# Kernel tuning notes

Measured on AMD Instinct MI355X. Metric: run time of the kernel, lower is better.

## Reference

```python
import jax, jax.numpy as jnp
import numpy as np

DIM = 192
HEADS = 8
EPS = 1e-12

def conv2d(x, w, groups=1, padding='SAME'):
    return jax.lax.conv_general_dilated(
        x, w, window_strides=(1, 1), padding=padding,
        dimension_numbers=('NCHW', 'OIHW', 'NCHW'),
        feature_group_count=groups)

def setup_inputs() -> dict:
    key = jax.random.key(0)
    ks = jax.random.split(key, 6)
    b, c, h, w = 8, DIM, 128, 128
    x = jax.random.normal(ks[0], (b, c, h, w), dtype=jnp.float32)
    # depthwise 3x3 conv on x (groups=dim): OIHW with I=1
    w_dw = jax.random.normal(ks[1], (DIM, 1, 3, 3), dtype=jnp.float32) * 0.1
    # 1x1 qkv projection
    w_qkv = jax.random.normal(ks[2], (DIM * 3, DIM, 1, 1), dtype=jnp.float32) * (1.0 / np.sqrt(DIM))
    # depthwise 3x3 on qkv (groups=3*dim)
    w_qkvdw = jax.random.normal(ks[3], (DIM * 3, 1, 3, 3), dtype=jnp.float32) * 0.1
    # 1x1 output projection
    w_proj = jax.random.normal(ks[4], (DIM, DIM, 1, 1), dtype=jnp.float32) * (1.0 / np.sqrt(DIM))
    temperature = jnp.ones((HEADS, 1, 1), dtype=jnp.float32)
    rescale = jnp.ones((HEADS, 1), dtype=jnp.float32)
    return {"x": x, "w_dw": w_dw, "w_qkv": w_qkv, "w_qkvdw": w_qkvdw,
            "w_proj": w_proj, "temperature": temperature, "rescale": rescale}

def l2norm_lastdim(t):
    # matches F.normalize(t, dim=-1, eps=1e-12)
    n = jnp.sqrt(jnp.sum(t * t, axis=-1, keepdims=True))
    return t / jnp.maximum(n, EPS)

def reference(x, w_dw, w_qkv, w_qkvdw, w_proj, temperature, rescale):
    b, c, h, w = x.shape
    heads = HEADS
    c_head = c // heads
    # variance (unbiased, like torch.var default) of depthwise-conv features over H,W
    xd = conv2d(x, w_dw, groups=c)                      # [b,c,h,w]
    var = jnp.var(xd, axis=(-2, -1), ddof=1)            # [b,c]
    var = var.reshape(b, heads, c_head)                 # [b,head,c_head]
    # qkv: 1x1 conv then depthwise 3x3
    qkv = conv2d(conv2d(x, w_qkv), w_qkvdw, groups=3 * c)  # [b,3c,h,w]
    q, k, v = jnp.split(qkv, 3, axis=1)
    def to_heads(t):
        return t.reshape(b, heads, c_head, h * w)       # b head c (h w)
    q, k, v = to_heads(q), to_heads(k), to_heads(v)
    q = l2norm_lastdim(q)
    k = l2norm_lastdim(k)
    # channel attention: [b,head,c_head,c_head]
    attn = jnp.einsum('bhcn,bhdn->bhcd', q, k) * temperature
    # diagonal bias from variance, scaled per-head
    diag = rescale * var                                # [b,head,c_head]
    attn = attn + jnp.einsum('bhc,cd->bhcd', diag, jnp.eye(c_head, dtype=attn.dtype))
    attn = jax.nn.softmax(attn, axis=-1)
    out = jnp.einsum('bhcd,bhdn->bhcn', attn, v)        # [b,head,c_head,hw]
    out = out.reshape(b, c, h, w)
    return conv2d(out, w_proj)
```

## Files before the change

### kernel.cpp

```cpp
#include <hip/hip_runtime.h>
#include <hip/hip_bf16.h>

typedef unsigned short ushort_t;
typedef __bf16 bf16x8 __attribute__((ext_vector_type(8)));
typedef float f32x4 __attribute__((ext_vector_type(4)));
typedef unsigned short us8 __attribute__((ext_vector_type(8)));
typedef unsigned short us4 __attribute__((ext_vector_type(4)));

#define HW 16384
#define CDIM 192
#define QKVC 576

static __device__ __forceinline__ float b2f(unsigned short u) {
    union { unsigned int i; float f; } cv; cv.i = ((unsigned int)u) << 16; return cv.f;
}
static __device__ __forceinline__ unsigned short f2b(float f) {
    union { __bf16 h; unsigned short u; } cv; cv.h = (__bf16)f; return cv.u;
}

__global__ __launch_bounds__(256) void k_cvt(const float* __restrict__ src,
                                             ushort_t* __restrict__ dst, int n8) {
    int i = blockIdx.x * 256 + threadIdx.x;
    if (i >= n8) return;
    f32x4 a = *(const f32x4*)&src[i * 8];
    f32x4 b = *(const f32x4*)&src[i * 8 + 4];
    us8 o;
#pragma unroll
    for (int e = 0; e < 4; ++e) { o[e] = f2b(a[e]); o[4 + e] = f2b(b[e]); }
    *(us8*)&dst[i * 8] = o;
}

__global__ __launch_bounds__(256) void k_dwvar(const float* __restrict__ x,
                                               const float* __restrict__ wdw,
                                               float* __restrict__ vs1,
                                               float* __restrict__ vs2,
                                               ushort_t* __restrict__ xb) {
    __shared__ __align__(16) float pl[66 * 132];
    __shared__ float red[8];
    int blk = blockIdx.x;
    int bc = blk >> 1, half = blk & 1, rb = half * 64;
    int c = bc % CDIM;
    const float* xp = x + (size_t)bc * HW;
    ushort_t* xbp = xb + (size_t)bc * HW;
    int t = threadIdx.x;
#pragma unroll
    for (int i = 0; i < 8; ++i) {
        int gi = t + i * 256;
        int row = gi >> 5, q4 = (gi & 31) * 4;
        f32x4 v4 = *(const f32x4*)&xp[(size_t)(rb + row) * 128 + q4];
        *(f32x4*)&pl[(row + 1) * 132 + q4] = v4;
        us4 b4;
#pragma unroll
        for (int j = 0; j < 4; ++j) b4[j] = f2b(v4[j]);
        *(us4*)&xbp[(size_t)(rb + row) * 128 + q4] = b4;
    }
    if (t < 32) {
        f32x4 v = {0.f, 0.f, 0.f, 0.f};
        if (rb > 0) v = *(const f32x4*)&xp[(size_t)(rb - 1) * 128 + t * 4];
        *(f32x4*)&pl[t * 4] = v;
    } else if (t < 64) {
        int g = t - 32;
        f32x4 v = {0.f, 0.f, 0.f, 0.f};
        if (rb + 64 < 128) v = *(const f32x4*)&xp[(size_t)(rb + 64) * 128 + g * 4];
        *(f32x4*)&pl[65 * 132 + g * 4] = v;
    }
    float w[9];
#pragma unroll
    for (int j = 0; j < 9; ++j) w[j] = wdw[c * 9 + j];
    __syncthreads();

    int lane = t & 63, wv = t >> 6;
    int y = lane, xs = wv * 32;
    int yb0 = y * 132, yb1 = yb0 + 132, yb2 = yb1 + 132;
    float l0 = 0.f, l1 = 0.f, l2 = 0.f;
    if (xs != 0) { l0 = pl[yb0 + xs - 1]; l1 = pl[yb1 + xs - 1]; l2 = pl[yb2 + xs - 1]; }
    float s1 = 0.f, s2 = 0.f;
#pragma unroll
    for (int g = 0; g < 4; ++g) {
        int x0 = xs + g * 8;
        float e0[10], e1[10], e2[10];
        e0[0] = l0; e1[0] = l1; e2[0] = l2;
        f32x4 a0 = *(const f32x4*)&pl[yb0 + x0], b0 = *(const f32x4*)&pl[yb0 + x0 + 4];
        f32x4 a1 = *(const f32x4*)&pl[yb1 + x0], b1 = *(const f32x4*)&pl[yb1 + x0 + 4];
        f32x4 a2 = *(const f32x4*)&pl[yb2 + x0], b2 = *(const f32x4*)&pl[yb2 + x0 + 4];
#pragma unroll
        for (int j = 0; j < 4; ++j) {
            e0[1 + j] = a0[j]; e0[5 + j] = b0[j];
            e1[1 + j] = a1[j]; e1[5 + j] = b1[j];
            e2[1 + j] = a2[j]; e2[5 + j] = b2[j];
        }
        float r0v = 0.f, r1v = 0.f, r2v = 0.f;
        if (x0 + 8 < 128) { r0v = pl[yb0 + x0 + 8]; r1v = pl[yb1 + x0 + 8]; r2v = pl[yb2 + x0 + 8]; }
        e0[9] = r0v; e1[9] = r1v; e2[9] = r2v;
#pragma unroll
        for (int j = 0; j < 8; ++j) {
            float o = e0[j] * w[0] + e0[j + 1] * w[1] + e0[j + 2] * w[2]
                    + e1[j] * w[3] + e1[j + 1] * w[4] + e1[j + 2] * w[5]
                    + e2[j] * w[6] + e2[j + 1] * w[7] + e2[j + 2] * w[8];
            s1 += o; s2 += o * o;
        }
        l0 = e0[8]; l1 = e1[8]; l2 = e2[8];
    }
#pragma unroll
    for (int off = 32; off; off >>= 1) { s1 += __shfl_xor(s1, off); s2 += __shfl_xor(s2, off); }
    if (lane == 0) { red[wv * 2] = s1; red[wv * 2 + 1] = s2; }
    __syncthreads();
    if (t == 0) {
        atomicAdd(&vs1[bc], red[0] + red[2] + red[4] + red[6]);
        atomicAdd(&vs2[bc], red[1] + red[3] + red[5] + red[7]);
    }
}

__global__ __launch_bounds__(256) void k_dwqkv(const ushort_t* __restrict__ qkvraw,
                                               const float* __restrict__ wqd,
                                               ushort_t* __restrict__ qkvd,
                                               float* __restrict__ ssq) {
    __shared__ __align__(16) ushort_t pl[66 * 136];
    __shared__ float red[4];
    int blk = blockIdx.x;
    int bo = blk >> 1, half = blk & 1, rb = half * 64;
    int o = bo % QKVC, b = bo / QKVC;
    const ushort_t* xp = qkvraw + (size_t)bo * HW;
    ushort_t* op = qkvd + (size_t)bo * HW;
    int t = threadIdx.x;
#pragma unroll
    for (int i = 0; i < 4; ++i) {
        int gi = t + i * 256;
        int row = gi >> 4, gr = (gi & 15) * 8;
        *(us8*)&pl[(row + 1) * 136 + gr] = *(const us8*)&xp[(size_t)(rb + row) * 128 + gr];
    }
    if (t < 16) {
        us8 v = {};
        if (rb > 0) v = *(const us8*)&xp[(size_t)(rb - 1) * 128 + t * 8];
        *(us8*)&pl[t * 8] = v;
    } else if (t < 32) {
        int g = t - 16;
        us8 v = {};
        if (rb + 64 < 128) v = *(const us8*)&xp[(size_t)(rb + 64) * 128 + g * 8];
        *(us8*)&pl[65 * 136 + g * 8] = v;
    }
    float w[9];
#pragma unroll
    for (int j = 0; j < 9; ++j) w[j] = wqd[o * 9 + j];
    __syncthreads();

    int lane = t & 63, wv = t >> 6;
    int y = lane, xs = wv * 32;
    int yb0 = y * 136, yb1 = yb0 + 136, yb2 = yb1 + 136;
    float l0 = 0.f, l1 = 0.f, l2 = 0.f;
    if (xs != 0) { l0 = b2f(pl[yb0 + xs - 1]); l1 = b2f(pl[yb1 + xs - 1]); l2 = b2f(pl[yb2 + xs - 1]); }
    float s2 = 0.f;
#pragma unroll
    for (int g = 0; g < 4; ++g) {
        int x0 = xs + g * 8;
        us8 v0 = *(const us8*)&pl[yb0 + x0];
        us8 v1 = *(const us8*)&pl[yb1 + x0];
        us8 v2 = *(const us8*)&pl[yb2 + x0];
        float r0v = 0.f, r1v = 0.f, r2v = 0.f;
        if (x0 + 8 < 128) { r0v = b2f(pl[yb0 + x0 + 8]); r1v = b2f(pl[yb1 + x0 + 8]); r2v = b2f(pl[yb2 + x0 + 8]); }
        float e0[10], e1[10], e2[10];
        e0[0] = l0; e1[0] = l1; e2[0] = l2;
#pragma unroll
        for (int j = 0; j < 8; ++j) { e0[j + 1] = b2f(v0[j]); e1[j + 1] = b2f(v1[j]); e2[j + 1] = b2f(v2[j]); }
        e0[9] = r0v; e1[9] = r1v; e2[9] = r2v;
        us8 ob;
#pragma unroll
        for (int j = 0; j < 8; ++j) {
            float ov = e0[j] * w[0] + e0[j + 1] * w[1] + e0[j + 2] * w[2]
                     + e1[j] * w[3] + e1[j + 1] * w[4] + e1[j + 2] * w[5]
                     + e2[j] * w[6] + e2[j + 1] * w[7] + e2[j + 2] * w[8];
            unsigned short bits = f2b(ov);
            ob[j] = bits;
            float rv = b2f(bits);
            s2 += rv * rv;
        }
        *(us8*)&op[(size_t)(rb + y) * 128 + x0] = ob;
        l0 = e0[8]; l1 = e1[8]; l2 = e2[8];
    }
#pragma unroll
    for (int off = 32; off; off >>= 1) s2 += __shfl_xor(s2, off);
    if (lane == 0) red[wv] = s2;
    __syncthreads();
    if (t == 0 && o < 2 * CDIM)
        atomicAdd(&ssq[b * 384 + o], red[0] + red[1] + red[2] + red[3]);
}

template<int CF>
__global__ __launch_bounds__(256) void k_gemm(const ushort_t* __restrict__ Av, long sAb,
                                              const ushort_t* __restrict__ Bv, long sBb,
                                              void* __restrict__ Cv, long sCb, int K) {
    __shared__ __align__(16) char smem[49152];
    ushort_t* As = (ushort_t*)smem;
    ushort_t* Bs = (ushort_t*)(smem + 24576);
    int t = threadIdx.x;
    int wv = t >> 6, lane = t & 63, quad = lane >> 4, l15 = lane & 15;
    size_t aoff = (size_t)blockIdx.z * sAb + (size_t)blockIdx.y * 192 * K;
    size_t boff = (size_t)blockIdx.z * sBb + (size_t)blockIdx.x * 128;
    size_t coff = (size_t)blockIdx.z * sCb + (size_t)blockIdx.y * 192 * HW + (size_t)blockIdx.x * 128;
    f32x4 acc[24] = {};
    int bkr = t >> 3, bn0 = (t & 7) * 16, tlow = t & 7;
    int gk0 = bkr >> 3, klo = bkr & 7;
    const ushort_t* Bp = Bv + boff;
    us8 pb0 = *(const us8*)&Bp[(size_t)bkr * HW + bn0];
    us8 pb1 = *(const us8*)&Bp[(size_t)bkr * HW + bn0 + 8];
    us8 pb2 = *(const us8*)&Bp[(size_t)(bkr + 32) * HW + bn0];
    us8 pb3 = *(const us8*)&Bp[(size_t)(bkr + 32) * HW + bn0 + 8];
    int nIter = K >> 6;
    for (int it = 0; it < nIter; ++it) {
        int kk = it << 6;
#pragma unroll
        for (int i = 0; i < 6; ++i) {
            int s = t + i * 256;
            int row = s >> 3, kc = (s & 7) * 8;
            int kcs = kc ^ ((row & 7) * 8);
            *(uint4*)&As[row * 64 + kcs] = *(const uint4*)&Av[aoff + (size_t)row * K + kk + kc];
        }
#pragma unroll
        for (int e = 0; e < 8; ++e) {
            int col0 = ((gk0 ^ tlow ^ e) << 3) + klo;
            Bs[(bn0 + e) * 64 + col0] = pb0[e];
            Bs[(bn0 + 8 + e) * 64 + col0] = pb1[e];
            int col1 = (((gk0 + 4) ^ tlow ^ e) << 3) + klo;
            Bs[(bn0 + e) * 64 + col1] = pb2[e];
            Bs[(bn0 + 8 + e) * 64 + col1] = pb3[e];
        }
        __syncthreads();
        if (it + 1 < nIter) {
            const ushort_t* Bn = &Bp[(size_t)(kk + 64) * HW];
            pb0 = *(const us8*)&Bn[(size_t)bkr * HW + bn0];
            pb1 = *(const us8*)&Bn[(size_t)bkr * HW + bn0 + 8];
            pb2 = *(const us8*)&Bn[(size_t)(bkr + 32) * HW + bn0];
            pb3 = *(const us8*)&Bn[(size_t)(bkr + 32) * HW + bn0 + 8];
        }
#pragma unroll
        for (int s = 0; s < 2; ++s) {
            int r0 = wv * 16 + l15, r1 = 64 + r0, r2 = 128 + r0;
            int ko = s * 32 + quad * 8;
            bf16x8 af0 = *(const bf16x8*)&As[r0 * 64 + (ko ^ ((r0 & 7) * 8))];
            bf16x8 af1 = *(const bf16x8*)&As[r1 * 64 + (ko ^ ((r1 & 7) * 8))];
            bf16x8 af2 = *(const bf16x8*)&As[r2 * 64 + (ko ^ ((r2 & 7) * 8))];
#pragma unroll
            for (int tc = 0; tc < 8; ++tc) {
                int n = tc * 16 + l15;
                int g = (s * 4 + quad) ^ ((tc ^ l15) & 7);
                bf16x8 bfr = *(const bf16x8*)&Bs[n * 64 + (g << 3)];
                acc[tc]      = __builtin_amdgcn_mfma_f32_16x16x32_bf16(af0, bfr, acc[tc],      0, 0, 0);
                acc[8 + tc]  = __builtin_amdgcn_mfma_f32_16x16x32_bf16(af1, bfr, acc[8 + tc],  0, 0, 0);
                acc[16 + tc] = __builtin_amdgcn_mfma_f32_16x16x32_bf16(af2, bfr, acc[16 + tc], 0, 0, 0);
            }
        }
        __syncthreads();
    }
    if (CF == 0) {
        ushort_t* Ct = (ushort_t*)smem;
#pragma unroll
        for (int rt = 0; rt < 3; ++rt)
#pragma unroll
            for (int tc = 0; tc < 8; ++tc)
#pragma unroll
                for (int r = 0; r < 4; ++r)
                    Ct[(rt * 64 + wv * 16 + quad * 4 + r) * 128 + tc * 16 + l15] = f2b(acc[rt * 8 + tc][r]);
        __syncthreads();
        ushort_t* Co = (ushort_t*)Cv;
#pragma unroll
        for (int i = 0; i < 12; ++i) {
            int s = t + i * 256;
            int row = s >> 4, c8 = (s & 15) * 8;
            *(us8*)&Co[coff + (size_t)row * HW + c8] = *(us8*)&Ct[row * 128 + c8];
        }
    } else {
        float* Cf = (float*)smem;
        float* Co = (float*)Cv;
#pragma unroll
        for (int rt = 0; rt < 3; ++rt) {
            if (rt) __syncthreads();
#pragma unroll
            for (int tc = 0; tc < 8; ++tc)
#pragma unroll
                for (int r = 0; r < 4; ++r)
                    Cf[(wv * 16 + quad * 4 + r) * 128 + tc * 16 + l15] = acc[rt * 8 + tc][r];
            __syncthreads();
#pragma unroll
            for (int i = 0; i < 8; ++i) {
                int s = t + i * 256;
                int row = s >> 5, c4 = (s & 31) * 4;
                *(f32x4*)&Co[coff + (size_t)(rt * 64 + row) * HW + c4] = *(f32x4*)&Cf[row * 128 + c4];
            }
        }
    }
}

__global__ __launch_bounds__(256) void k_gram(const ushort_t* __restrict__ qkvd,
                                              float* __restrict__ G) {
    __shared__ __align__(16) ushort_t qs[24 * 264];
    __shared__ __align__(16) ushort_t ks[24 * 264];
    int bh = blockIdx.y;
    int b = bh >> 3, h = bh & 7;
    int t = threadIdx.x, wv = t >> 6, lane = t & 63, quad = lane >> 4, l15 = lane & 15;
    const ushort_t* qb = qkvd + (size_t)b * 9437184 + (size_t)(h * 24) * HW;
    const ushort_t* kp = qb + (size_t)CDIM * HW;
    f32x4 a00 = {}, a01 = {}, a10 = {}, a11 = {};
    bf16x8 z = {};
    bool hi = (l15 < 8);
    int kbase0 = blockIdx.x * 2048;
    for (int sub = 0; sub < 8; ++sub) {
        int kbase = kbase0 + sub * 256;
#pragma unroll
        for (int j = 0; j < 3; ++j) {
            int gi = t + j * 256;
            int row = gi >> 5, c8 = (gi & 31) * 8;
            *(us8*)&qs[row * 264 + c8] = *(const us8*)&qb[(size_t)row * HW + kbase + c8];
            *(us8*)&ks[row * 264 + c8] = *(const us8*)&kp[(size_t)row * HW + kbase + c8];
        }
        __syncthreads();
#pragma unroll
        for (int s = 0; s < 2; ++s) {
            int ko = (wv * 2 + s) * 32 + quad * 8;
            bf16x8 qa0 = *(const bf16x8*)&qs[l15 * 264 + ko];
            bf16x8 qa1 = hi ? *(const bf16x8*)&qs[(16 + l15) * 264 + ko] : z;
            bf16x8 kb0 = *(const bf16x8*)&ks[l15 * 264 + ko];
            bf16x8 kb1 = hi ? *(const bf16x8*)&ks[(16 + l15) * 264 + ko] : z;
            a00 = __builtin_amdgcn_mfma_f32_16x16x32_bf16(qa0, kb0, a00, 0, 0, 0);
            a01 = __builtin_amdgcn_mfma_f32_16x16x32_bf16(qa0, kb1, a01, 0, 0, 0);
            a10 = __builtin_amdgcn_mfma_f32_16x16x32_bf16(qa1, kb0, a10, 0, 0, 0);
            a11 = __builtin_amdgcn_mfma_f32_16x16x32_bf16(qa1, kb1, a11, 0, 0, 0);
        }
        __syncthreads();
    }
    float* Gp = G + (size_t)bh * 576;
#pragma unroll
    for (int r = 0; r < 4; ++r) {
        int r0 = quad * 4 + r, r1 = 16 + quad * 4 + r;
        int c0 = l15, c1 = 16 + l15;
        atomicAdd(&Gp[r0 * 24 + c0], a00[r]);
        if (c1 < 24) atomicAdd(&Gp[r0 * 24 + c1], a01[r]);
        if (r1 < 24) atomicAdd(&Gp[r1 * 24 + c0], a10[r]);
        if (r1 < 24 && c1 < 24) atomicAdd(&Gp[r1 * 24 + c1], a11[r]);
    }
}

__global__ __launch_bounds__(256) void k_smweff(const float* __restrict__ G,
                                                const float* __restrict__ ssq,
                                                const float* __restrict__ vs1,
                                                const float* __restrict__ vs2,
                                                const float* __restrict__ wproj,
                                                const float* __restrict__ temp,
                                                const float* __restrict__ resc,
                                                ushort_t* __restrict__ Weff) {
    int b = blockIdx.x, t = threadIdx.x;
    __shared__ float P[8 * 24 * 24];
    __shared__ float snq[192], snk[192];
    if (t < 192) {
        snq[t] = fmaxf(sqrtf(ssq[b * 384 + t]), 1e-12f);
        snk[t] = fmaxf(sqrtf(ssq[b * 384 + 192 + t]), 1e-12f);
    }
    __syncthreads();
    if (t < 192) {
        int h = t / 24, c = t % 24;
        float tmpv = temp[h];
        float S1 = vs1[b * 192 + t], S2 = vs2[b * 192 + t];
        float varv = (S2 - S1 * S1 * (1.0f / 16384.f)) * (1.0f / 16383.f);
        float dvar = resc[h] * varv;
        const float* Gp = G + (size_t)(b * 8 + h) * 576 + c * 24;
        float inq = tmpv / snq[t];
        float lg[24]; float mx = -1e30f;
#pragma unroll
        for (int d = 0; d < 24; ++d) {
            float v = Gp[d] * inq / snk[h * 24 + d];
            if (d == c) v += dvar;
            lg[d] = v; mx = fmaxf(mx, v);
        }
        float sum = 0.f;
#pragma unroll
        for (int d = 0; d < 24; ++d) { float e = __expf(lg[d] - mx); lg[d] = e; sum += e; }
        float inv = 1.f / sum;
#pragma unroll
        for (int d = 0; d < 24; ++d) P[(h * 24 + c) * 24 + d] = lg[d] * inv;
    }
    __syncthreads();
#pragma unroll
    for (int i = 0; i < 6; ++i) {
        int idx = t + (blockIdx.y * 6 + i) * 256;
        int co = idx / 192, hd = idx % 192;
        int h2 = hd / 24, d = hd % 24;
        float a = 0.f;
#pragma unroll
        for (int c2 = 0; c2 < 24; ++c2)
            a += wproj[co * 192 + h2 * 24 + c2] * P[(h2 * 24 + c2) * 24 + d];
        Weff[(size_t)b * 36864 + idx] = f2b(a);
    }
}

extern "C" void kernel_launch(void* const* d_in, const int* in_sizes, int n_in,
                              void* d_out, int out_size, void* d_ws, size_t ws_size,
                              hipStream_t stream) {
    const float* x      = (const float*)d_in[0];
    const float* wdw    = (const float*)d_in[1];
    const float* wqkv   = (const float*)d_in[2];
    const float* wqkvdw = (const float*)d_in[3];
    const float* wproj  = (const float*)d_in[4];
    const float* temp   = (const float*)d_in[5];
    const float* resc   = (const float*)d_in[6];
    float* out = (float*)d_out;

    char* ws = (char*)d_ws;
    ushort_t* qkvraw = (ushort_t*)ws;
    ushort_t* qkvd   = (ushort_t*)(ws + 150994944);
    char* small = ws + 301989888;
    float* vs1  = (float*)small;
    float* vs2  = (float*)(small + 6144);
    float* ssq  = (float*)(small + 12288);
    float* G    = (float*)(small + 24576);
    ushort_t* Weff = (ushort_t*)(small + 172032);

    ushort_t* xb  = qkvd;
    ushort_t* wqb = qkvd + 60000000;

    (void)hipMemsetAsync(small, 0, 172032, stream);
    k_cvt<<<dim3(54), dim3(256), 0, stream>>>(wqkv, wqb, 13824);
    k_dwvar<<<dim3(3072), dim3(256), 0, stream>>>(x, wdw, vs1, vs2, xb);
    k_gemm<0><<<dim3(128, 3, 8), dim3(256), 0, stream>>>(wqb, 0L, xb, 3145728L, qkvraw, 9437184L, 192);
    k_dwqkv<<<dim3(9216), dim3(256), 0, stream>>>(qkvraw, wqkvdw, qkvd, ssq);
    k_gram<<<dim3(8, 64), dim3(256), 0, stream>>>(qkvd, G);
    k_smweff<<<dim3(8, 24), dim3(256), 0, stream>>>(G, ssq, vs1, vs2, wproj, temp, resc, Weff);
    k_gemm<1><<<dim3(128, 1, 8), dim3(256), 0, stream>>>(Weff, 36864L, qkvd + (size_t)384 * HW, 9437184L, out, 3145728L, 192);
}
```

Baseline: 365.1 us.

## Replace LDS-staged depthwise convs with register/shuffle halos and smaller tiles

Both depthwise 3x3 kernels (variance pass and qkv pass) drop the shared-memory plane staging and __syncthreads. Each thread now loads its three rows of 8 columns straight from global memory and gets left/right halo values from neighbouring lanes via shuffles. Blocks now cover 16 rows instead of 64, giving 4x more blocks, and each wavefront issues its own atomicAdd. This removes LDS traffic and barriers but reads each input row three times from global/L2. It also multiplies the number of atomics, and the qkv sum of squares now uses the unrounded fp32 value instead of the bf16-rounded one.

New measurement: 404.7 us. +10.8%, slower.

```diff
diff --git a/kernel.cpp b/kernel.cpp
--- a/kernel.cpp
+++ b/kernel.cpp
@@ -35,154 +35,108 @@
                                                float* __restrict__ vs1,
                                                float* __restrict__ vs2,
                                                ushort_t* __restrict__ xb) {
-    __shared__ __align__(16) float pl[66 * 132];
-    __shared__ float red[8];
-    int blk = blockIdx.x;
-    int bc = blk >> 1, half = blk & 1, rb = half * 64;
+    int bc = blockIdx.x >> 3;
+    int rb = (blockIdx.x & 7) << 4;
     int c = bc % CDIM;
+    int t = threadIdx.x;
+    int l15 = t & 15;
+    int r = rb + (t >> 4);
+    int c0 = l15 * 8;
     const float* xp = x + (size_t)bc * HW;
     ushort_t* xbp = xb + (size_t)bc * HW;
-    int t = threadIdx.x;
-#pragma unroll
-    for (int i = 0; i < 8; ++i) {
-        int gi = t + i * 256;
-        int row = gi >> 5, q4 = (gi & 31) * 4;
-        f32x4 v4 = *(const f32x4*)&xp[(size_t)(rb + row) * 128 + q4];
-        *(f32x4*)&pl[(row + 1) * 132 + q4] = v4;
-        us4 b4;
-#pragma unroll
-        for (int j = 0; j < 4; ++j) b4[j] = f2b(v4[j]);
-        *(us4*)&xbp[(size_t)(rb + row) * 128 + q4] = b4;
-    }
-    if (t < 32) {
-        f32x4 v = {0.f, 0.f, 0.f, 0.f};
-        if (rb > 0) v = *(const f32x4*)&xp[(size_t)(rb - 1) * 128 + t * 4];
-        *(f32x4*)&pl[t * 4] = v;
-    } else if (t < 64) {
-        int g = t - 32;
-        f32x4 v = {0.f, 0.f, 0.f, 0.f};
-        if (rb + 64 < 128) v = *(const f32x4*)&xp[(size_t)(rb + 64) * 128 + g * 4];
-        *(f32x4*)&pl[65 * 132 + g * 4] = v;
-    }
     float w[9];
 #pragma unroll
     for (int j = 0; j < 9; ++j) w[j] = wdw[c * 9 + j];
-    __syncthreads();
-
-    int lane = t & 63, wv = t >> 6;
-    int y = lane, xs = wv * 32;
-    int yb0 = y * 132, yb1 = yb0 + 132, yb2 = yb1 + 132;
-    float l0 = 0.f, l1 = 0.f, l2 = 0.f;
-    if (xs != 0) { l0 = pl[yb0 + xs - 1]; l1 = pl[yb1 + xs - 1]; l2 = pl[yb2 + xs - 1]; }
+
+    f32x4 z4 = {0.f, 0.f, 0.f, 0.f};
+    f32x4 a0, b0, a1, b1, a2, b2;
+    if (r > 0) { a0 = *(const f32x4*)&xp[(size_t)(r - 1) * 128 + c0];
+                 b0 = *(const f32x4*)&xp[(size_t)(r - 1) * 128 + c0 + 4]; }
+    else       { a0 = z4; b0 = z4; }
+    a1 = *(const f32x4*)&xp[(size_t)r * 128 + c0];
+    b1 = *(const f32x4*)&xp[(size_t)r * 128 + c0 + 4];
+    if (r < 127) { a2 = *(const f32x4*)&xp[(size_t)(r + 1) * 128 + c0];
+                   b2 = *(const f32x4*)&xp[(size_t)(r + 1) * 128 + c0 + 4]; }
+    else         { a2 = z4; b2 = z4; }
+
+    us8 xo;
+#pragma unroll
+    for (int j = 0; j < 4; ++j) { xo[j] = f2b(a1[j]); xo[4 + j] = f2b(b1[j]); }
+    *(us8*)&xbp[(size_t)r * 128 + c0] = xo;
+
+    float e0[10], e1[10], e2[10];
+#pragma unroll
+    for (int j = 0; j < 4; ++j) {
+        e0[1 + j] = a0[j]; e0[5 + j] = b0[j];
+        e1[1 + j] = a1[j]; e1[5 + j] = b1[j];
+        e2[1 + j] = a2[j]; e2[5 + j] = b2[j];
+    }
+    float u0 = __shfl_up(e0[8], 1), u1 = __shfl_up(e1[8], 1), u2 = __shfl_up(e2[8], 1);
+    float d0 = __shfl_down(e0[1], 1), d1 = __shfl_down(e1[1], 1), d2 = __shfl_down(e2[1], 1);
+    bool le = (l15 == 0), re = (l15 == 15);
+    e0[0] = le ? 0.f : u0; e1[0] = le ? 0.f : u1; e2[0] = le ? 0.f : u2;
+    e0[9] = re ? 0.f : d0; e1[9] = re ? 0.f : d1; e2[9] = re ? 0.f : d2;
+
     float s1 = 0.f, s2 = 0.f;
 #pragma unroll
-    for (int g = 0; g < 4; ++g) {
-        int x0 = xs + g * 8;
-        float e0[10], e1[10], e2[10];
-        e0[0] = l0; e1[0] = l1; e2[0] = l2;
-        f32x4 a0 = *(const f32x4*)&pl[yb0 + x0], b0 = *(const f32x4*)&pl[yb0 + x0 + 4];
-        f32x4 a1 = *(const f32x4*)&pl[yb1 + x0], b1 = *(const f32x4*)&pl[yb1 + x0 + 4];
-        f32x4 a2 = *(const f32x4*)&pl[yb2 + x0], b2 = *(const f32x4*)&pl[yb2 + x0 + 4];
-#pragma unroll
-        for (int j = 0; j < 4; ++j) {
-            e0[1 + j] = a0[j]; e0[5 + j] = b0[j];
-            e1[1 + j] = a1[j]; e1[5 + j] = b1[j];
-            e2[1 + j] = a2[j]; e2[5 + j] = b2[j];
-        }
-        float r0v = 0.f, r1v = 0.f, r2v = 0.f;
-        if (x0 + 8 < 128) { r0v = pl[yb0 + x0 + 8]; r1v = pl[yb1 + x0 + 8]; r2v = pl[yb2 + x0 + 8]; }
-        e0[9] = r0v; e1[9] = r1v; e2[9] = r2v;
-#pragma unroll
-        for (int j = 0; j < 8; ++j) {
-            float o = e0[j] * w[0] + e0[j + 1] * w[1] + e0[j + 2] * w[2]
-                    + e1[j] * w[3] + e1[j + 1] * w[4] + e1[j + 2] * w[5]
-                    + e2[j] * w[6] + e2[j + 1] * w[7] + e2[j + 2] * w[8];
-            s1 += o; s2 += o * o;
-        }
-        l0 = e0[8]; l1 = e1[8]; l2 = e2[8];
+    for (int j = 0; j < 8; ++j) {
+        float o = e0[j] * w[0] + e0[j + 1] * w[1] + e0[j + 2] * w[2]
+                + e1[j] * w[3] + e1[j + 1] * w[4] + e1[j + 2] * w[5]
+                + e2[j] * w[6] + e2[j + 1] * w[7] + e2[j + 2] * w[8];
+        s1 += o; s2 += o * o;
     }
 #pragma unroll
     for (int off = 32; off; off >>= 1) { s1 += __shfl_xor(s1, off); s2 += __shfl_xor(s2, off); }
-    if (lane == 0) { red[wv * 2] = s1; red[wv * 2 + 1] = s2; }
-    __syncthreads();
-    if (t == 0) {
-        atomicAdd(&vs1[bc], red[0] + red[2] + red[4] + red[6]);
-        atomicAdd(&vs2[bc], red[1] + red[3] + red[5] + red[7]);
-    }
+    if ((t & 63) == 0) { atomicAdd(&vs1[bc], s1); atomicAdd(&vs2[bc], s2); }
 }
 
 __global__ __launch_bounds__(256) void k_dwqkv(const ushort_t* __restrict__ qkvraw,
                                                const float* __restrict__ wqd,
                                                ushort_t* __restrict__ qkvd,
                                                float* __restrict__ ssq) {
-    __shared__ __align__(16) ushort_t pl[66 * 136];
-    __shared__ float red[4];
-    int blk = blockIdx.x;
-    int bo = blk >> 1, half = blk & 1, rb = half * 64;
+    int bo = blockIdx.x >> 3;
+    int rb = (blockIdx.x & 7) << 4;
     int o = bo % QKVC, b = bo / QKVC;
+    int t = threadIdx.x;
+    int l15 = t & 15;
+    int r = rb + (t >> 4);
+    int c0 = l15 * 8;
     const ushort_t* xp = qkvraw + (size_t)bo * HW;
     ushort_t* op = qkvd + (size_t)bo * HW;
-    int t = threadIdx.x;
-#pragma unroll
-    for (int i = 0; i < 4; ++i) {
-        int gi = t + i * 256;
-        int row = gi >> 4, gr = (gi & 15) * 8;
-        *(us8*)&pl[(row + 1) * 136 + gr] = *(const us8*)&xp[(size_t)(rb + row) * 128 + gr];
-    }
-    if (t < 16) {
-        us8 v = {};
-        if (rb > 0) v = *(const us8*)&xp[(size_t)(rb - 1) * 128 + t * 8];
-        *(us8*)&pl[t * 8] = v;
-    } else if (t < 32) {
-        int g = t - 16;
-        us8 v = {};
-        if (rb + 64 < 128) v = *(const us8*)&xp[(size_t)(rb + 64) * 128 + g * 8];
-        *(us8*)&pl[65 * 136 + g * 8] = v;
-    }
     float w[9];
 #pragma unroll
     for (int j = 0; j < 9; ++j) w[j] = wqd[o * 9 + j];
-    __syncthreads();
-
-    int lane = t & 63, wv = t >> 6;
-    int y = lane, xs = wv * 32;
-    int yb0 = y * 136, yb1 = yb0 + 136, yb2 = yb1 + 136;
-    float l0 = 0.f, l1 = 0.f, l2 = 0.f;
-    if (xs != 0) { l0 = b2f(pl[yb0 + xs - 1]); l1 = b2f(pl[yb1 + xs - 1]); l2 = b2f(pl[yb2 + xs - 1]); }
+
+    us8 zv = {};
+    us8 v0 = (r > 0)   ? *(const us8*)&xp[(size_t)(r - 1) * 128 + c0] : zv;
+    us8 v1 =             *(const us8*)&xp[(size_t)r * 128 + c0];
+    us8 v2 = (r < 127) ? *(const us8*)&xp[(size_t)(r + 1) * 128 + c0] : zv;
+
+    float e0[10], e1[10], e2[10];
+#pragma unroll
+    for (int j = 0; j < 8; ++j) { e0[j + 1] = b2f(v0[j]); e1[j + 1] = b2f(v1[j]); e2[j + 1] = b2f(v2[j]); }
+    float u0 = __shfl_up(e0[8], 1), u1 = __shfl_up(e1[8], 1), u2 = __shfl_up(e2[8], 1);
+    float d0 = __shfl_down(e0[1], 1), d1 = __shfl_down(e1[1], 1), d2 = __shfl_down(e2[1], 1);
+    bool le = (l15 == 0), re = (l15 == 15);
+    e0[0] = le ? 0.f : u0; e1[0] = le ? 0.f : u1; e2[0] = le ? 0.f : u2;
+    e0[9] = re ? 0.f : d0; e1[9] = re ? 0.f : d1; e2[9] = re ? 0.f : d2;
+
+    us8 ob;
     float s2 = 0.f;
 #pragma unroll
-    for (int g = 0; g < 4; ++g) {
-        int x0 = xs + g * 8;
-        us8 v0 = *(const us8*)&pl[yb0 + x0];
-        us8 v1 = *(const us8*)&pl[yb1 + x0];
-        us8 v2 = *(const us8*)&pl[yb2 + x0];
-        float r0v = 0.f, r1v = 0.f, r2v = 0.f;
-        if (x0 + 8 < 128) { r0v = b2f(pl[yb0 + x0 + 8]); r1v = b2f(pl[yb1 + x0 + 8]); r2v = b2f(pl[yb2 + x0 + 8]); }
-        float e0[10], e1[10], e2[10];
-        e0[0] = l0; e1[0] = l1; e2[0] = l2;
-#pragma unroll
-        for (int j = 0; j < 8; ++j) { e0[j + 1] = b2f(v0[j]); e1[j + 1] = b2f(v1[j]); e2[j + 1] = b2f(v2[j]); }
-        e0[9] = r0v; e1[9] = r1v; e2[9] = r2v;
-        us8 ob;
-#pragma unroll
-        for (int j = 0; j < 8; ++j) {
-            float ov = e0[j] * w[0] + e0[j + 1] * w[1] + e0[j + 2] * w[2]
-                     + e1[j] * w[3] + e1[j + 1] * w[4] + e1[j + 2] * w[5]
-                     + e2[j] * w[6] + e2[j + 1] * w[7] + e2[j + 2] * w[8];
-            unsigned short bits = f2b(ov);
-            ob[j] = bits;
-            float rv = b2f(bits);
-            s2 += rv * rv;
-        }
-        *(us8*)&op[(size_t)(rb + y) * 128 + x0] = ob;
-        l0 = e0[8]; l1 = e1[8]; l2 = e2[8];
-    }
-#pragma unroll
-    for (int off = 32; off; off >>= 1) s2 += __shfl_xor(s2, off);
-    if (lane == 0) red[wv] = s2;
-    __syncthreads();
-    if (t == 0 && o < 2 * CDIM)
-        atomicAdd(&ssq[b * 384 + o], red[0] + red[1] + red[2] + red[3]);
+    for (int j = 0; j < 8; ++j) {
+        float ov = e0[j] * w[0] + e0[j + 1] * w[1] + e0[j + 2] * w[2]
+                 + e1[j] * w[3] + e1[j + 1] * w[4] + e1[j + 2] * w[5]
+                 + e2[j] * w[6] + e2[j + 1] * w[7] + e2[j + 2] * w[8];
+        ob[j] = f2b(ov);
+        s2 += ov * ov;
+    }
+    *(us8*)&op[(size_t)r * 128 + c0] = ob;
+    if (o < 2 * CDIM) {
+#pragma unroll
+        for (int off = 32; off; off >>= 1) s2 += __shfl_xor(s2, off);
+        if ((t & 63) == 0) atomicAdd(&ssq[b * 384 + o], s2);
+    }
 }
 
 template<int CF>
@@ -418,9 +372,9 @@
 
     (void)hipMemsetAsync(small, 0, 172032, stream);
     k_cvt<<<dim3(54), dim3(256), 0, stream>>>(wqkv, wqb, 13824);
-    k_dwvar<<<dim3(3072), dim3(256), 0, stream>>>(x, wdw, vs1, vs2, xb);
+    k_dwvar<<<dim3(12288), dim3(256), 0, stream>>>(x, wdw, vs1, vs2, xb);
     k_gemm<0><<<dim3(128, 3, 8), dim3(256), 0, stream>>>(wqb, 0L, xb, 3145728L, qkvraw, 9437184L, 192);
-    k_dwqkv<<<dim3(9216), dim3(256), 0, stream>>>(qkvraw, wqkvdw, qkvd, ssq);
+    k_dwqkv<<<dim3(36864), dim3(256), 0, stream>>>(qkvraw, wqkvdw, qkvd, ssq);
     k_gram<<<dim3(8, 64), dim3(256), 0, stream>>>(qkvd, G);
     k_smweff<<<dim3(8, 24), dim3(256), 0, stream>>>(G, ssq, vs1, vs2, wproj, temp, resc, Weff);
     k_gemm<1><<<dim3(128, 1, 8), dim3(256), 0, stream>>>(Weff, 36864L, qkvd + (size_t)384 * HW, 9437184L, out, 3145728L, 192);
```
